# Optimization experiments

Hardware: AMD Instinct MI355X
Metric: run time of the kernel (lower is better)

The kernel has to match this reference:

```python
import jax, jax.numpy as jnp
import numpy as np

# ---- module hyperparameters (match BlurredNoise defaults) ----
CHANNELS = 1024
BLUR_WIDTHS = 128
NOISE_CHANNELS = CHANNELS // BLUR_WIDTHS  # 8
MIN_SR = 250.0
MAX_SR = 10000.0
CUTOFF = 2.0
WIDTH = 12.0
SR_BASE = 2.0
NORM_PER_FILTER = 1.0
KERNEL_SIZE = int(np.ceil(MAX_SR / 2))  # 5000

BATCH = 2
SEQ_LENGTH = 4096
IN_SEQ = SEQ_LENGTH + KERNEL_SIZE - 1  # 9095


def _kaiser_beta(a):
    # scipy.signal.kaiser_beta
    if a > 50:
        return 0.1102 * (a - 8.7)
    if a > 21:
        return 0.5842 * (a - 21) ** 0.4 + 0.07886 * (a - 21)
    return 0.0


def _firwin_lowpass(numtaps, cutoff, width, fs):
    # Re-implementation of scipy.signal.firwin(numtaps, cutoff, width=width, fs=fs)
    # (lowpass, pass_zero=True, Kaiser window chosen from transition width).
    nyq = 0.5 * fs
    atten = 2.285 * (numtaps - 1) * np.pi * (width / nyq) + 7.95  # kaiser_atten
    beta = _kaiser_beta(atten)
    win = np.kaiser(numtaps, beta)
    m = np.arange(numtaps) - (numtaps - 1) / 2.0
    right = cutoff / nyq
    h = right * np.sinc(right * m)  # ideal lowpass impulse response
    h = h * win
    h = h / h.sum()  # normalize DC gain to 1 (scale at f=0, pass_zero)
    return h.astype(np.float32)


def _build_filters():
    log_min = np.log(MIN_SR) / np.log(SR_BASE)
    log_max = np.log(MAX_SR) / np.log(SR_BASE)
    sampling_rates = SR_BASE ** np.linspace(log_min, log_max, BLUR_WIDTHS)
    sampling_rates = np.clip(sampling_rates, MIN_SR, MAX_SR)
    blur_filters = np.zeros((BLUR_WIDTHS, KERNEL_SIZE), dtype=np.float32)
    for i, sr in enumerate(sampling_rates):
        num_taps = int(np.ceil(sr / 2))
        blur_filters[i, -num_taps:] = _firwin_lowpass(num_taps, CUTOFF, WIDTH, sr)
    output_scale = 1.0 / np.sqrt((blur_filters ** 2).sum(axis=1))  # (128,)
    output_scale = output_scale.reshape(1, BLUR_WIDTHS, 1).astype(np.float32)
    return blur_filters, output_scale


def setup_inputs() -> dict:
    key = jax.random.key(0)
    noise = jax.random.normal(key, (BATCH, NOISE_CHANNELS, IN_SEQ), dtype=jnp.float32)
    bf, os_ = _build_filters()
    return {
        "noise": noise,
        "blur_filters": jnp.asarray(bf),
        "output_scale": jnp.asarray(os_),
    }


def reference(noise, blur_filters, output_scale):
    # noise: (n, c, t_in) with c = NOISE_CHANNELS
    n, c, t = noise.shape
    # einops.repeat 'n c t -> (n c) b t' followed by grouped conv (groups=b)
    # with per-group single input channel is exactly a standard conv with
    # 1 input channel and b output channels.
    x = noise.reshape(n * c, 1, t)                       # (n*c, 1, t_in)
    k = blur_filters[:, None, :]                         # (b, 1, K) OIW
    feats = jax.lax.conv_general_dilated(
        x, k, window_strides=(1,), padding="VALID",
        dimension_numbers=("NCH", "OIH", "NCH"))          # (n*c, b, T)
    feats = feats * (1.0 + NORM_PER_FILTER * (output_scale - 1.0))
    T = feats.shape[-1]
    # '(n c) b t -> n (c b) t'
    return feats.reshape(n, c * BLUR_WIDTHS, T)
```

## Files before the change

kernel.cpp:

```cpp
#include <hip/hip_runtime.h>
#include <hip/hip_bf16.h>


#define KS      5000
#define IN_SEQ  9095
#define T_OUT   4096
#define NBC     16
#define NF      128
#define NSTEP   157
#define SWZSTEP 176
#define CSTRIDE 1056
#define XBUF    (4*CSTRIDE)
#define XPS     9344
#define SWZ_BYTES (8*SWZSTEP*512*2)
#define MT      2

typedef __attribute__((ext_vector_type(8))) short v8s;
typedef __attribute__((ext_vector_type(4))) float v4f;

__device__ __forceinline__ unsigned short f2b(float v) {
  union { __hip_bfloat16 h; unsigned short u; } cv;
  cv.h = __float2bfloat16(v);
  return cv.u;
}

__global__ void build_pre(const float* __restrict__ filt,
                          const float* __restrict__ noise,
                          unsigned short* __restrict__ swz,
                          float* __restrict__ xpad) {
  const int b = blockIdx.x;
  if (b < 314) {
    const int i = b * 256 + threadIdx.x;
    if (i >= 8 * NSTEP * 64) return;
    const int n  = i & 15;
    const int q  = (i >> 4) & 3;
    const int sb = i >> 6;
    const int ft = sb / NSTEP;
    const int s  = sb - ft * NSTEP;
    const int jg0 = KS - 32 * (s + 1) + 8 * q;
    const float* row = filt + (size_t)(ft * 16 + n) * KS;
    unsigned short o[8];
    #pragma unroll
    for (int j = 0; j < 8; ++j) {
      int jg = jg0 + j;
      int jc = jg < 0 ? 0 : jg;
      float v = (jg >= 0) ? row[jc] : 0.0f;
      o[j] = f2b(v);
    }
    *(uint4*)(swz + (((size_t)(ft * SWZSTEP + s)) << 9) + (q << 7) + (n << 3)) = *(uint4*)o;
  } else {
    const int i = (b - 314) * 256 + threadIdx.x;
    if (i >= NBC * XPS) return;
    const int r = i / XPS;
    const int pcol = i - r * XPS;
    const int lg = pcol - 32;
    xpad[i] = (lg >= 0 && lg < IN_SEQ) ? noise[r * IN_SEQ + lg] : 0.0f;
  }
}

template<int W, int U, int NG, int SB, int D>
__device__ __forceinline__ void run_seg(
    const char* __restrict__ bb, const float* __restrict__ xn,
    char* xb, int xrd_off, int t0, int lane, v4f (&acc)[MT][8])
{
  v8s breg[D][W];
  v8s areg[2][MT];
  float4 xr[3];
  const char* xrd = xb + xrd_off;

  const char* sp[W];
  #pragma unroll
  for (int w = 0; w < W; ++w)
    sp[w] = bb + (((size_t)((8 - W + w) * SWZSTEP + SB)) << 10);

  auto stage_load = [&](int gg) {
    const int g0 = t0 + KS - 32 * (SB + (gg + 1) * U);
    #pragma unroll
    for (int ii = 0; ii < 3; ++ii)
      xr[ii] = *(const float4*)(xn + (g0 + 8 * lane + 4 * ii));
  };
  auto stage_write = [&](int parity) {
    const float* f = (const float*)xr;
    unsigned u6[6];
    #pragma unroll
    for (int j = 0; j < 6; ++j)
      u6[j] = (unsigned)f2b(f[2 * j]) | ((unsigned)f2b(f[2 * j + 1]) << 16);
    auto AL = [](unsigned hi, unsigned lo) { return (lo >> 16) | (hi << 16); };
    char* buf = xb + parity * XBUF + 16 * lane;
    uint4 w0 = {u6[0], u6[1], u6[2], u6[3]};
    uint4 w1 = {AL(u6[1],u6[0]), AL(u6[2],u6[1]), AL(u6[3],u6[2]), AL(u6[4],u6[3])};
    uint4 w2 = {u6[1], u6[2], u6[3], u6[4]};
    uint4 w3 = {AL(u6[2],u6[1]), AL(u6[3],u6[2]), AL(u6[4],u6[3]), AL(u6[5],u6[4])};
    *(uint4*)(buf + 0 * CSTRIDE) = w0;
    *(uint4*)(buf + 1 * CSTRIDE) = w1;
    *(uint4*)(buf + 2 * CSTRIDE) = w2;
    *(uint4*)(buf + 3 * CSTRIDE) = w3;
  };
  auto read_A = [&](const char* p, v8s (&dst)[MT]) {
    #pragma unroll
    for (int mt = 0; mt < MT; ++mt) {
      v8s a;
      *(uint2*)&a       = *(const uint2*)(p + 32 * mt);
      *((uint2*)&a + 1) = *(const uint2*)(p + 32 * mt + 8);
      dst[mt] = a;
    }
  };

  #pragma unroll
  for (int d = 0; d < D; ++d)
    #pragma unroll
    for (int w = 0; w < W; ++w)
      breg[d][w] = *(const v8s*)(sp[w] + (d << 10));
  stage_load(0);
  stage_write(0);
  stage_load(NG > 1 ? 1 : 0);
  read_A(xrd + 64 * (U - 1), areg[0]);

  #pragma unroll 1
  for (int g = 0; g < NG; ++g) {
    #pragma unroll
    for (int i = 0; i < U; ++i) {
      if (i == 1) stage_write((g + 1) & 1);
      if (i == 2) { int gg = g + 2; gg = gg > NG - 1 ? NG - 1 : gg; stage_load(gg); }
      {
        const char* pn;
        if (i + 1 < U) {
          pn = xrd + (g & 1) * XBUF + 64 * (U - 2 - i);
        } else {
          int gn = (g + 1 < NG) ? (g + 1) : g;
          pn = xrd + (gn & 1) * XBUF + 64 * (U - 1);
        }
        read_A(pn, areg[(i + 1) & 1]);
      }
      #pragma unroll
      for (int w = 0; w < W; ++w)
        #pragma unroll
        for (int mt = 0; mt < MT; ++mt)
          acc[mt][8 - W + w] = __builtin_amdgcn_mfma_f32_16x16x32_bf16(
              areg[i & 1][mt], breg[i % D][w], acc[mt][8 - W + w], 0, 0, 0);
      #pragma unroll
      for (int w = 0; w < W; ++w)
        breg[i % D][w] = *(const v8s*)(sp[w] + ((i + D) << 10));
    }
    #pragma unroll
    for (int w = 0; w < W; ++w) sp[w] += (U << 10);
  }
}

__global__ __launch_bounds__(64, 2) void blur_mfma(
    const float* __restrict__ xpad,
    const unsigned short* __restrict__ swz,
    const float* __restrict__ scale,
    float* __restrict__ out)
{
  __shared__ __align__(16) char xb[2 * XBUF];
  const int lane = threadIdx.x;
  const int b  = blockIdx.x;
  const int bc = b >> 7;
  const int t0 = (b & 127) << 5;
  const int m = lane & 15, q = lane >> 4, c = m & 3;
  const float* __restrict__ xn = xpad + (size_t)bc * XPS + 32;
  const char* bb = (const char*)swz + 16 * lane;
  const int xrd_off = c * CSTRIDE + 8 * (m >> 2) + 16 * q;

  v4f acc[MT][8];
  const v4f vz = {0.f, 0.f, 0.f, 0.f};
  #pragma unroll
  for (int mt = 0; mt < MT; ++mt)
    #pragma unroll
    for (int n = 0; n < 8; ++n) acc[mt][n] = vz;

  run_seg<8,  8, 1,   0,  2>(bb, xn, xb, xrd_off, t0, lane, acc);
  run_seg<7,  4, 1,   8,  2>(bb, xn, xb, xrd_off, t0, lane, acc);
  run_seg<6,  4, 1,  12,  2>(bb, xn, xb, xrd_off, t0, lane, acc);
  run_seg<5, 12, 1,  16,  3>(bb, xn, xb, xrd_off, t0, lane, acc);
  run_seg<4, 12, 1,  28,  4>(bb, xn, xb, xrd_off, t0, lane, acc);
  run_seg<3, 12, 2,  40,  6>(bb, xn, xb, xrd_off, t0, lane, acc);
  run_seg<2, 12, 3,  64,  6>(bb, xn, xb, xrd_off, t0, lane, acc);
  run_seg<1, 12, 4, 100, 12>(bb, xn, xb, xrd_off, t0, lane, acc);
  run_seg<1,  9, 1, 148,  9>(bb, xn, xb, xrd_off, t0, lane, acc);

  #pragma unroll
  for (int n = 0; n < 8; ++n) {
    const int F = 16 * n + m;
    const float sc = scale[F];
    #pragma unroll
    for (int mt = 0; mt < MT; ++mt) {
      v4f o = acc[mt][n] * sc;
      *(v4f*)(out + (size_t)(bc * NF + F) * T_OUT + t0 + 16 * mt + 4 * q) = o;
    }
  }
}

extern "C" void kernel_launch(void* const* d_in, const int* in_sizes, int n_in,
                              void* d_out, int out_size, void* d_ws, size_t ws_size,
                              hipStream_t stream) {
  const float* noise = (const float*)d_in[0];
  const float* filt  = (const float*)d_in[1];
  const float* scale = (const float*)d_in[2];
  float* out = (float*)d_out;

  unsigned short* swz = (unsigned short*)d_ws;
  float* xpad = (float*)((char*)d_ws + SWZ_BYTES);

  const int pad_blocks = (NBC * XPS + 255) / 256;
  build_pre<<<314 + pad_blocks, 256, 0, stream>>>(filt, noise, swz, xpad);
  blur_mfma<<<2048, 64, 0, stream>>>(xpad, swz, scale, out);
}
```

Before: 118.4 us.

## Share filter tiles across four waves via double-buffered LDS staging

Blocks grow from one wave to four, each wave handling a different 32-sample time slice of the same channel. Filter B-tiles are now loaded cooperatively once per block into a double-buffered LDS chunk and read by all four waves, instead of each wave streaming them from global memory. The segment schedule is re-tuned to smaller U and D so a group fits the 16KB chunk. The cost is a __syncthreads per group and extra LDS traffic and pressure, which may lower occupancy. The padded input buffer gains a zeroed tail to cover the new reads.

After: 409.8 us. 246% more time.

```diff
diff --git a/kernel.cpp b/kernel.cpp
--- a/kernel.cpp
+++ b/kernel.cpp
@@ -12,8 +12,12 @@
 #define CSTRIDE 1056
 #define XBUF    (4*CSTRIDE)
 #define XPS     9344
+#define XTAIL   256
 #define SWZ_BYTES (8*SWZSTEP*512*2)
 #define MT      2
+#define CHUNK   16384
+#define XREG    (2*XBUF)
+#define BOFF    (4*XREG)
 
 typedef __attribute__((ext_vector_type(8))) short v8s;
 typedef __attribute__((ext_vector_type(4))) float v4f;
@@ -50,28 +54,57 @@
     *(uint4*)(swz + (((size_t)(ft * SWZSTEP + s)) << 9) + (q << 7) + (n << 3)) = *(uint4*)o;
   } else {
     const int i = (b - 314) * 256 + threadIdx.x;
-    if (i >= NBC * XPS) return;
+    if (i >= NBC * XPS + XTAIL) return;
     const int r = i / XPS;
     const int pcol = i - r * XPS;
     const int lg = pcol - 32;
-    xpad[i] = (lg >= 0 && lg < IN_SEQ) ? noise[r * IN_SEQ + lg] : 0.0f;
+    xpad[i] = (r < NBC && lg >= 0 && lg < IN_SEQ) ? noise[r * IN_SEQ + lg] : 0.0f;
   }
 }
 
 template<int W, int U, int NG, int SB, int D>
 __device__ __forceinline__ void run_seg(
-    const char* __restrict__ bb, const float* __restrict__ xn,
-    char* xb, int xrd_off, int t0, int lane, v4f (&acc)[MT][8])
+    const char* __restrict__ swzg, const float* __restrict__ xn,
+    char* lds, int xrd_off, int t0, int lane, int wid, v4f (&acc)[MT][8])
 {
+  constexpr int TILES = W * U;
+  constexpr int TPW   = (TILES + 3) / 4;
+  constexpr int LOADI = (U >= 3) ? 2 : 1;
+  constexpr int ODD   = U & 1;
+
+  char* xw  = lds + wid * XREG;
+  char* bB  = lds + BOFF;
+  const char* xrd = xw + xrd_off;
+
   v8s breg[D][W];
   v8s areg[2][MT];
   float4 xr[3];
-  const char* xrd = xb + xrd_off;
-
-  const char* sp[W];
-  #pragma unroll
-  for (int w = 0; w < W; ++w)
-    sp[w] = bb + (((size_t)((8 - W + w) * SWZSTEP + SB)) << 10);
+  uint4 bstg[TPW];
+
+  auto loadB = [&](int g) {
+    #pragma unroll
+    for (int j = 0; j < TPW; ++j) {
+      const int tile = wid * TPW + j;
+      if (tile < TILES) {
+        const int wp = tile / U;
+        const int u  = tile - wp * U;
+        const int s  = SB + g * U + u;
+        bstg[j] = *(const uint4*)(swzg +
+            (((size_t)((8 - W + wp) * SWZSTEP + s)) << 10) + 16 * lane);
+      }
+    }
+  };
+  auto writeB = [&](int par) {
+    #pragma unroll
+    for (int j = 0; j < TPW; ++j) {
+      const int tile = wid * TPW + j;
+      if (tile < TILES)
+        *(uint4*)(bB + par * CHUNK + (tile << 10) + 16 * lane) = bstg[j];
+    }
+  };
+  auto readB = [&](int par, int w, int step) -> v8s {
+    return *(const v8s*)(bB + par * CHUNK + ((w * U + step) << 10) + 16 * lane);
+  };
 
   auto stage_load = [&](int gg) {
     const int g0 = t0 + KS - 32 * (SB + (gg + 1) * U);
@@ -86,7 +119,7 @@
     for (int j = 0; j < 6; ++j)
       u6[j] = (unsigned)f2b(f[2 * j]) | ((unsigned)f2b(f[2 * j + 1]) << 16);
     auto AL = [](unsigned hi, unsigned lo) { return (lo >> 16) | (hi << 16); };
-    char* buf = xb + parity * XBUF + 16 * lane;
+    char* buf = xw + parity * XBUF + 16 * lane;
     uint4 w0 = {u6[0], u6[1], u6[2], u6[3]};
     uint4 w1 = {AL(u6[1],u6[0]), AL(u6[2],u6[1]), AL(u6[3],u6[2]), AL(u6[4],u6[3])};
     uint4 w2 = {u6[1], u6[2], u6[3], u6[4]};
@@ -106,22 +139,27 @@
     }
   };
 
-  #pragma unroll
-  for (int d = 0; d < D; ++d)
-    #pragma unroll
-    for (int w = 0; w < W; ++w)
-      breg[d][w] = *(const v8s*)(sp[w] + (d << 10));
+  loadB(0);
   stage_load(0);
   stage_write(0);
   stage_load(NG > 1 ? 1 : 0);
+  writeB(0);
+  __syncthreads();
   read_A(xrd + 64 * (U - 1), areg[0]);
 
   #pragma unroll 1
   for (int g = 0; g < NG; ++g) {
+    if (g + 1 < NG) loadB(g + 1);
+    #pragma unroll
+    for (int d = 0; d < D; ++d)
+      #pragma unroll
+      for (int w = 0; w < W; ++w)
+        breg[d][w] = readB(g & 1, w, d);
     #pragma unroll
     for (int i = 0; i < U; ++i) {
+      const int ap = ((ODD ? g : 0) + i) & 1;
       if (i == 1) stage_write((g + 1) & 1);
-      if (i == 2) { int gg = g + 2; gg = gg > NG - 1 ? NG - 1 : gg; stage_load(gg); }
+      if (i == LOADI) { int gg = g + 2; gg = gg > NG - 1 ? NG - 1 : gg; stage_load(gg); }
       {
         const char* pn;
         if (i + 1 < U) {
@@ -130,37 +168,41 @@
           int gn = (g + 1 < NG) ? (g + 1) : g;
           pn = xrd + (gn & 1) * XBUF + 64 * (U - 1);
         }
-        read_A(pn, areg[(i + 1) & 1]);
+        read_A(pn, areg[ap ^ 1]);
       }
       #pragma unroll
       for (int w = 0; w < W; ++w)
         #pragma unroll
         for (int mt = 0; mt < MT; ++mt)
           acc[mt][8 - W + w] = __builtin_amdgcn_mfma_f32_16x16x32_bf16(
-              areg[i & 1][mt], breg[i % D][w], acc[mt][8 - W + w], 0, 0, 0);
-      #pragma unroll
-      for (int w = 0; w < W; ++w)
-        breg[i % D][w] = *(const v8s*)(sp[w] + ((i + D) << 10));
-    }
-    #pragma unroll
-    for (int w = 0; w < W; ++w) sp[w] += (U << 10);
+              areg[ap][mt], breg[i % D][w], acc[mt][8 - W + w], 0, 0, 0);
+      if (i + D < U) {
+        #pragma unroll
+        for (int w = 0; w < W; ++w)
+          breg[i % D][w] = readB(g & 1, w, i + D);
+      }
+    }
+    if (g + 1 < NG) writeB((g + 1) & 1);
+    __syncthreads();
   }
 }
 
-__global__ __launch_bounds__(64, 2) void blur_mfma(
+__global__ __launch_bounds__(256, 2) void blur_mfma(
     const float* __restrict__ xpad,
     const unsigned short* __restrict__ swz,
     const float* __restrict__ scale,
     float* __restrict__ out)
 {
-  __shared__ __align__(16) char xb[2 * XBUF];
-  const int lane = threadIdx.x;
+  __shared__ __align__(16) char lds[BOFF + 2 * CHUNK];
+  const int tid  = threadIdx.x;
+  const int lane = tid & 63;
+  const int wid  = tid >> 6;
   const int b  = blockIdx.x;
-  const int bc = b >> 7;
-  const int t0 = (b & 127) << 5;
+  const int bc = b >> 5;
+  const int t0 = ((b & 31) << 7) + (wid << 5);
   const int m = lane & 15, q = lane >> 4, c = m & 3;
   const float* __restrict__ xn = xpad + (size_t)bc * XPS + 32;
-  const char* bb = (const char*)swz + 16 * lane;
+  const char* swzg = (const char*)swz;
   const int xrd_off = c * CSTRIDE + 8 * (m >> 2) + 16 * q;
 
   v4f acc[MT][8];
@@ -170,15 +212,15 @@
     #pragma unroll
     for (int n = 0; n < 8; ++n) acc[mt][n] = vz;
 
-  run_seg<8,  8, 1,   0,  2>(bb, xn, xb, xrd_off, t0, lane, acc);
-  run_seg<7,  4, 1,   8,  2>(bb, xn, xb, xrd_off, t0, lane, acc);
-  run_seg<6,  4, 1,  12,  2>(bb, xn, xb, xrd_off, t0, lane, acc);
-  run_seg<5, 12, 1,  16,  3>(bb, xn, xb, xrd_off, t0, lane, acc);
-  run_seg<4, 12, 1,  28,  4>(bb, xn, xb, xrd_off, t0, lane, acc);
-  run_seg<3, 12, 2,  40,  6>(bb, xn, xb, xrd_off, t0, lane, acc);
-  run_seg<2, 12, 3,  64,  6>(bb, xn, xb, xrd_off, t0, lane, acc);
-  run_seg<1, 12, 4, 100, 12>(bb, xn, xb, xrd_off, t0, lane, acc);
-  run_seg<1,  9, 1, 148,  9>(bb, xn, xb, xrd_off, t0, lane, acc);
+  run_seg<8,  2, 4,   0, 1>(swzg, xn, lds, xrd_off, t0, lane, wid, acc);
+  run_seg<7,  2, 2,   8, 1>(swzg, xn, lds, xrd_off, t0, lane, wid, acc);
+  run_seg<6,  2, 2,  12, 1>(swzg, xn, lds, xrd_off, t0, lane, wid, acc);
+  run_seg<5,  3, 4,  16, 1>(swzg, xn, lds, xrd_off, t0, lane, wid, acc);
+  run_seg<4,  4, 3,  28, 1>(swzg, xn, lds, xrd_off, t0, lane, wid, acc);
+  run_seg<3,  4, 6,  40, 2>(swzg, xn, lds, xrd_off, t0, lane, wid, acc);
+  run_seg<2,  6, 6,  64, 2>(swzg, xn, lds, xrd_off, t0, lane, wid, acc);
+  run_seg<1, 12, 4, 100, 4>(swzg, xn, lds, xrd_off, t0, lane, wid, acc);
+  run_seg<1,  9, 1, 148, 3>(swzg, xn, lds, xrd_off, t0, lane, wid, acc);
 
   #pragma unroll
   for (int n = 0; n < 8; ++n) {
@@ -203,7 +245,7 @@
   unsigned short* swz = (unsigned short*)d_ws;
   float* xpad = (float*)((char*)d_ws + SWZ_BYTES);
 
-  const int pad_blocks = (NBC * XPS + 255) / 256;
+  const int pad_blocks = (NBC * XPS + XTAIL + 255) / 256;
   build_pre<<<314 + pad_blocks, 256, 0, stream>>>(filt, noise, swz, xpad);
-  blur_mfma<<<2048, 64, 0, stream>>>(xpad, swz, scale, out);
-}
+  blur_mfma<<<512, 256, 0, stream>>>(xpad, swz, scale, out);
+}
```
